# Performance work log

Hardware: AMD Instinct MI355X
Metric: run time of the kernel (lower is better)

The kernel has to match this reference:

```python
import jax, jax.numpy as jnp
import numpy as np

K_MAX = 3
ITERS = 3
NEG_BIG = -1e9


def squash(x):
    # x: [..., O]
    sn = jnp.sum(jnp.square(x), axis=-1, keepdims=True)
    factor = sn / (1.0 + sn) / jnp.sqrt(sn + 1e-8)
    return factor * x


def setup_inputs() -> dict:
    key = jax.random.key(0)
    k1, k2, k3, k4 = jax.random.split(key, 4)
    N, L, D, O = 4096, 200, 64, 64
    behavior_embs = jax.random.normal(k1, (N, L, D), dtype=jnp.float32)
    W = jax.random.normal(k2, (D, O), dtype=jnp.float32)  # init_std=1.0
    routing_logits_init = jax.random.normal(k3, (N, K_MAX, L), dtype=jnp.float32)
    seq_len = jax.random.randint(k4, (N, 1), 0, L, dtype=jnp.int32)
    return {
        "behavior_embs": behavior_embs,
        "W": W,
        "routing_logits_init": routing_logits_init,
        "seq_len": seq_len,
    }


def reference(behavior_embs, W, routing_logits_init, seq_len):
    N, L, D = behavior_embs.shape
    # mask: [N, K_MAX, L] -- valid positions along L, tiled across capsules
    mask = jnp.arange(L)[None, None, :] < seq_len[:, None, :]  # [N,1,L]
    mask = jnp.broadcast_to(mask, (N, K_MAX, L))

    mappings = jnp.matmul(behavior_embs, W)          # [N, L, O]
    m_det = jax.lax.stop_gradient(mappings)         # routing uses detached mappings

    logits = routing_logits_init                     # [N, K_MAX, L]
    for _ in range(ITERS - 1):
        padded = jnp.where(mask, logits, NEG_BIG)
        # NOTE: softmax over the capsule dim (axis=1), as in the original
        weights = jax.nn.softmax(padded, axis=1)     # [N, K_MAX, L]
        candidates = jnp.matmul(weights, m_det)      # [N, K_MAX, O]
        interests = squash(candidates)
        logits = logits + jnp.einsum('nko,nlo->nkl', interests, m_det)

    padded = jnp.where(mask, logits, NEG_BIG)
    weights = jax.nn.softmax(padded, axis=1)
    candidates = jnp.matmul(weights, mappings)       # final iter uses non-detached
    interests = squash(candidates)                   # [N, K_MAX, O]
    return interests
```

## Files before the change

kernel.cpp:

```cpp
#include <hip/hip_runtime.h>
#include <math.h>

typedef _Float16 f16;
typedef _Float16 f16x8 __attribute__((ext_vector_type(8)));
typedef float f32x4 __attribute__((ext_vector_type(4)));

#define LSEQ 200
#define LT 13
#define LKS 7
#define WSTRIDE 224
#define ISTRIDE 80

__global__ __launch_bounds__(256, 4)
void capsule_kernel(const float* __restrict__ E,
                    const float* __restrict__ W,
                    const float* __restrict__ RL,
                    const int* __restrict__ SL,
                    float* __restrict__ out)
{
    __shared__ f16 m_sw[LT*2*64*8];
    __shared__ f16 w_c[3*WSTRIDE];
    __shared__ f16 i_c[3*ISTRIDE];
    __shared__ float logits[3*LSEQ];
    __shared__ float cand[3*64];

    const int n = blockIdx.x;
    const int t = threadIdx.x;
    const int lane = t & 63;
    const int wv = t >> 6;
    const int q = lane >> 4;
    const int cc = lane & 15;

    const int o_own = wv*16 + cc;
    f16x8 wB[2];
    #pragma unroll
    for (int ks = 0; ks < 2; ks++) {
        f16x8 h;
        #pragma unroll
        for (int j = 0; j < 8; j++) h[j] = (f16)W[(ks*32 + q*8 + j)*64 + o_own];
        wB[ks] = h;
    }

    const float4 f4z = make_float4(0.f, 0.f, 0.f, 0.f);

    const float* Eb = E + (size_t)n * (LSEQ*64);
    for (int g = t; g < LT*2*64; g += 256) {
        int sb = g >> 6, c = g & 63;
        int Tl = sb >> 1, ks = sb & 1;
        int qq = c >> 4, m = c & 15;
        int l = Tl*16 + m;
        int kb = ks*32 + qq*8;
        float4 v0 = f4z, v1 = f4z;
        if (l < LSEQ) {
            v0 = *(const float4*)(Eb + l*64 + kb);
            v1 = *(const float4*)(Eb + l*64 + kb + 4);
        }
        f16x8 h = { (f16)v0.x,(f16)v0.y,(f16)v0.z,(f16)v0.w,
                    (f16)v1.x,(f16)v1.y,(f16)v1.z,(f16)v1.w };
        *(f16x8*)&m_sw[g*8] = h;
    }

    if (t < 150) {
        float4 v = *(const float4*)(RL + (size_t)n * 600 + t*4);
        *(float4*)&logits[t*4] = v;
    }
    const int s = SL[n];

    __syncthreads();

    f32x4 acc[LT];
    #pragma unroll
    for (int Tl = 0; Tl < LT; Tl++) {
        f32x4 c0 = {0.f, 0.f, 0.f, 0.f};
        #pragma unroll
        for (int ks = 0; ks < 2; ks++) {
            f16x8 a = *(f16x8*)&m_sw[((Tl*2 + ks)*64 + lane)*8];
            c0 = __builtin_amdgcn_mfma_f32_16x16x32_f16(a, wB[ks], c0, 0, 0, 0);
        }
        acc[Tl] = c0;
    }
    __syncthreads();

    const int kso = o_own >> 5, qo = (o_own & 31) >> 3, jo = o_own & 7;
    #pragma unroll
    for (int Tl = 0; Tl < LT; Tl++) {
        #pragma unroll
        for (int r = 0; r < 4; r++) {
            int lp = q*4 + r;
            m_sw[((Tl*2 + kso)*64 + qo*16 + lp)*8 + jo] = (f16)acc[Tl][r];
        }
    }
    __syncthreads();

    f16x8 mfrag[LKS];
    #pragma unroll
    for (int ks = 0; ks < LKS; ks++) {
        f16x8 h;
        #pragma unroll
        for (int j = 0; j < 8; j++) {
            int l = ks*32 + q*8 + j;
            f16 v = (f16)0.f;
            if (l < 208) {
                int Tl = l >> 4, lp = l & 15;
                v = m_sw[((Tl*2 + kso)*64 + qo*16 + lp)*8 + jo];
            }
            h[j] = v;
        }
        mfrag[ks] = h;
    }

    if (t < LSEQ) {
        float w0, w1, w2;
        if (t < s) {
            float l0 = logits[t], l1 = logits[LSEQ + t], l2 = logits[2*LSEQ + t];
            float mx = fmaxf(fmaxf(l0, l1), l2);
            float e0 = expf(l0 - mx), e1 = expf(l1 - mx), e2 = expf(l2 - mx);
            float inv = 1.f / (e0 + e1 + e2);
            w0 = e0*inv; w1 = e1*inv; w2 = e2*inv;
        } else {
            w0 = w1 = w2 = (1.f/3.f);
        }
        w_c[t]             = (f16)w0;
        w_c[WSTRIDE + t]   = (f16)w1;
        w_c[2*WSTRIDE + t] = (f16)w2;
    }
    __syncthreads();

    const f16x8 hz = {(f16)0.f,(f16)0.f,(f16)0.f,(f16)0.f,
                      (f16)0.f,(f16)0.f,(f16)0.f,(f16)0.f};

    for (int iter = 0; iter < 3; iter++) {
        f32x4 ca = {0.f, 0.f, 0.f, 0.f};
        #pragma unroll
        for (int ks = 0; ks < LKS; ks++) {
            f16x8 b = hz;
            if (cc < 3) b = *(f16x8*)&w_c[cc*WSTRIDE + ks*32 + q*8];
            ca = __builtin_amdgcn_mfma_f32_16x16x32_f16(mfrag[ks], b, ca, 0, 0, 0);
        }
        if (cc < 3) {
            #pragma unroll
            for (int r = 0; r < 4; r++) cand[cc*64 + wv*16 + q*4 + r] = ca[r];
        }
        __syncthreads();

        if (t < 192) {
            float x = cand[t];
            float sq = x*x;
            #pragma unroll
            for (int off = 32; off >= 1; off >>= 1) sq += __shfl_xor(sq, off, 64);
            float factor = sq / ((1.f + sq) * sqrtf(sq + 1e-8f));
            float y = factor * x;
            if (iter < 2) {
                int k = t >> 6, o = t & 63;
                i_c[k*ISTRIDE + o] = (f16)y;
            } else {
                out[(size_t)n*192 + t] = y;
            }
        }
        if (iter == 2) break;
        __syncthreads();

        for (int Tn = wv; Tn < LT; Tn += 4) {
            f32x4 da = {0.f, 0.f, 0.f, 0.f};
            #pragma unroll
            for (int ko = 0; ko < 2; ko++) {
                f16x8 a = hz;
                if (cc < 3) a = *(f16x8*)&i_c[cc*ISTRIDE + ko*32 + q*8];
                f16x8 b = *(f16x8*)&m_sw[((Tn*2 + ko)*64 + lane)*8];
                da = __builtin_amdgcn_mfma_f32_16x16x32_f16(a, b, da, 0, 0, 0);
            }
            if (lane < 16) {
                int l = Tn*16 + lane;
                if (l < LSEQ) {
                    float w0, w1, w2;
                    if (l < s) {
                        float l0 = logits[l]          + da[0];
                        float l1 = logits[LSEQ + l]   + da[1];
                        float l2 = logits[2*LSEQ + l] + da[2];
                        logits[l] = l0; logits[LSEQ + l] = l1; logits[2*LSEQ + l] = l2;
                        float mx = fmaxf(fmaxf(l0, l1), l2);
                        float e0 = expf(l0 - mx), e1 = expf(l1 - mx), e2 = expf(l2 - mx);
                        float inv = 1.f / (e0 + e1 + e2);
                        w0 = e0*inv; w1 = e1*inv; w2 = e2*inv;
                    } else {
                        w0 = w1 = w2 = (1.f/3.f);
                    }
                    w_c[l]             = (f16)w0;
                    w_c[WSTRIDE + l]   = (f16)w1;
                    w_c[2*WSTRIDE + l] = (f16)w2;
                }
            }
        }
        __syncthreads();
    }
}

extern "C" void kernel_launch(void* const* d_in, const int* in_sizes, int n_in,
                              void* d_out, int out_size, void* d_ws, size_t ws_size,
                              hipStream_t stream) {
    const float* E  = (const float*)d_in[0];
    const float* W  = (const float*)d_in[1];
    const float* RL = (const float*)d_in[2];
    const int*   SL = (const int*)d_in[3];
    float* o = (float*)d_out;
    const int N = in_sizes[3];
    capsule_kernel<<<dim3(N), dim3(256), 0, stream>>>(E, W, RL, SL, o);
}
```

Baseline: 314.6 us.

## Keep routing logits in registers and raise occupancy to five blocks per CU

```diff
diff --git a/kernel.cpp b/kernel.cpp
--- a/kernel.cpp
+++ b/kernel.cpp
@@ -7,22 +7,18 @@
 
 #define LSEQ 200
 #define LT 13
-#define LKS 7
-#define WSTRIDE 224
-#define ISTRIDE 80
-
-__global__ __launch_bounds__(256, 4)
+
+__global__ __launch_bounds__(256, 5)
 void capsule_kernel(const float* __restrict__ E,
                     const float* __restrict__ W,
                     const float* __restrict__ RL,
                     const int* __restrict__ SL,
                     float* __restrict__ out)
 {
-    __shared__ f16 m_sw[LT*2*64*8];
-    __shared__ f16 w_c[3*WSTRIDE];
-    __shared__ f16 i_c[3*ISTRIDE];
-    __shared__ float logits[3*LSEQ];
-    __shared__ float cand[3*64];
+    __shared__ f16 m_sw[1792*8];
+    __shared__ f16 w_c[3*224];
+    __shared__ f16 i_c[3*80];
+    __shared__ float cand[192];
 
     const int n = blockIdx.x;
     const int t = threadIdx.x;
@@ -30,6 +26,7 @@
     const int wv = t >> 6;
     const int q = lane >> 4;
     const int cc = lane & 15;
+    const int cmin = cc < 3 ? cc : 2;
 
     const int o_own = wv*16 + cc;
     f16x8 wB[2];
@@ -41,10 +38,33 @@
         wB[ks] = h;
     }
 
+    float lg[4][3];
+    #pragma unroll
+    for (int slot = 0; slot < 4; slot++) {
+        int Tn = wv + slot*4;
+        if (Tn < LT && lane < 16) {
+            int l = Tn*16 + lane;
+            if (l < LSEQ) {
+                lg[slot][0] = RL[(size_t)n*600 + l];
+                lg[slot][1] = RL[(size_t)n*600 + 200 + l];
+                lg[slot][2] = RL[(size_t)n*600 + 400 + l];
+            }
+        }
+    }
+    const int s = SL[n];
+
+    if (t < 9) {
+        const f16x8 hz = {(f16)0.f,(f16)0.f,(f16)0.f,(f16)0.f,
+                          (f16)0.f,(f16)0.f,(f16)0.f,(f16)0.f};
+        int row = t / 3, off = 200 + (t % 3)*8;
+        *(f16x8*)&w_c[row*224 + off] = hz;
+    }
+
+    const float* Eb = E + (size_t)n * (LSEQ*64);
     const float4 f4z = make_float4(0.f, 0.f, 0.f, 0.f);
-
-    const float* Eb = E + (size_t)n * (LSEQ*64);
-    for (int g = t; g < LT*2*64; g += 256) {
+    #pragma unroll
+    for (int i = 0; i < 7; i++) {
+        int g = t + i*256;
         int sb = g >> 6, c = g & 63;
         int Tl = sb >> 1, ks = sb & 1;
         int qq = c >> 4, m = c & 15;
@@ -60,12 +80,6 @@
         *(f16x8*)&m_sw[g*8] = h;
     }
 
-    if (t < 150) {
-        float4 v = *(const float4*)(RL + (size_t)n * 600 + t*4);
-        *(float4*)&logits[t*4] = v;
-    }
-    const int s = SL[n];
-
     __syncthreads();
 
     f32x4 acc[LT];
@@ -90,11 +104,33 @@
             m_sw[((Tl*2 + kso)*64 + qo*16 + lp)*8 + jo] = (f16)acc[Tl][r];
         }
     }
+    #pragma unroll
+    for (int slot = 0; slot < 4; slot++) {
+        int Tn = wv + slot*4;
+        if (Tn < LT && lane < 16) {
+            int l = Tn*16 + lane;
+            if (l < LSEQ) {
+                float w0, w1, w2;
+                if (l < s) {
+                    float l0 = lg[slot][0], l1 = lg[slot][1], l2 = lg[slot][2];
+                    float mx = fmaxf(fmaxf(l0, l1), l2);
+                    float e0 = expf(l0 - mx), e1 = expf(l1 - mx), e2 = expf(l2 - mx);
+                    float inv = 1.f / (e0 + e1 + e2);
+                    w0 = e0*inv; w1 = e1*inv; w2 = e2*inv;
+                } else {
+                    w0 = w1 = w2 = (1.f/3.f);
+                }
+                w_c[l]       = (f16)w0;
+                w_c[224 + l] = (f16)w1;
+                w_c[448 + l] = (f16)w2;
+            }
+        }
+    }
     __syncthreads();
 
-    f16x8 mfrag[LKS];
-    #pragma unroll
-    for (int ks = 0; ks < LKS; ks++) {
+    f16x8 mfrag[7];
+    #pragma unroll
+    for (int ks = 0; ks < 7; ks++) {
         f16x8 h;
         #pragma unroll
         for (int j = 0; j < 8; j++) {
@@ -109,32 +145,11 @@
         mfrag[ks] = h;
     }
 
-    if (t < LSEQ) {
-        float w0, w1, w2;
-        if (t < s) {
-            float l0 = logits[t], l1 = logits[LSEQ + t], l2 = logits[2*LSEQ + t];
-            float mx = fmaxf(fmaxf(l0, l1), l2);
-            float e0 = expf(l0 - mx), e1 = expf(l1 - mx), e2 = expf(l2 - mx);
-            float inv = 1.f / (e0 + e1 + e2);
-            w0 = e0*inv; w1 = e1*inv; w2 = e2*inv;
-        } else {
-            w0 = w1 = w2 = (1.f/3.f);
-        }
-        w_c[t]             = (f16)w0;
-        w_c[WSTRIDE + t]   = (f16)w1;
-        w_c[2*WSTRIDE + t] = (f16)w2;
-    }
-    __syncthreads();
-
-    const f16x8 hz = {(f16)0.f,(f16)0.f,(f16)0.f,(f16)0.f,
-                      (f16)0.f,(f16)0.f,(f16)0.f,(f16)0.f};
-
     for (int iter = 0; iter < 3; iter++) {
         f32x4 ca = {0.f, 0.f, 0.f, 0.f};
         #pragma unroll
-        for (int ks = 0; ks < LKS; ks++) {
-            f16x8 b = hz;
-            if (cc < 3) b = *(f16x8*)&w_c[cc*WSTRIDE + ks*32 + q*8];
+        for (int ks = 0; ks < 7; ks++) {
+            f16x8 b = *(f16x8*)&w_c[cmin*224 + ks*32 + q*8];
             ca = __builtin_amdgcn_mfma_f32_16x16x32_f16(mfrag[ks], b, ca, 0, 0, 0);
         }
         if (cc < 3) {
@@ -151,8 +166,7 @@
             float factor = sq / ((1.f + sq) * sqrtf(sq + 1e-8f));
             float y = factor * x;
             if (iter < 2) {
-                int k = t >> 6, o = t & 63;
-                i_c[k*ISTRIDE + o] = (f16)y;
+                i_c[(t >> 6)*80 + (t & 63)] = (f16)y;
             } else {
                 out[(size_t)n*192 + t] = y;
             }
@@ -160,34 +174,39 @@
         if (iter == 2) break;
         __syncthreads();
 
-        for (int Tn = wv; Tn < LT; Tn += 4) {
-            f32x4 da = {0.f, 0.f, 0.f, 0.f};
-            #pragma unroll
-            for (int ko = 0; ko < 2; ko++) {
-                f16x8 a = hz;
-                if (cc < 3) a = *(f16x8*)&i_c[cc*ISTRIDE + ko*32 + q*8];
-                f16x8 b = *(f16x8*)&m_sw[((Tn*2 + ko)*64 + lane)*8];
-                da = __builtin_amdgcn_mfma_f32_16x16x32_f16(a, b, da, 0, 0, 0);
-            }
-            if (lane < 16) {
-                int l = Tn*16 + lane;
-                if (l < LSEQ) {
-                    float w0, w1, w2;
-                    if (l < s) {
-                        float l0 = logits[l]          + da[0];
-                        float l1 = logits[LSEQ + l]   + da[1];
-                        float l2 = logits[2*LSEQ + l] + da[2];
-                        logits[l] = l0; logits[LSEQ + l] = l1; logits[2*LSEQ + l] = l2;
-                        float mx = fmaxf(fmaxf(l0, l1), l2);
-                        float e0 = expf(l0 - mx), e1 = expf(l1 - mx), e2 = expf(l2 - mx);
-                        float inv = 1.f / (e0 + e1 + e2);
-                        w0 = e0*inv; w1 = e1*inv; w2 = e2*inv;
-                    } else {
-                        w0 = w1 = w2 = (1.f/3.f);
+        f16x8 ia[2];
+        ia[0] = *(f16x8*)&i_c[cmin*80 + q*8];
+        ia[1] = *(f16x8*)&i_c[cmin*80 + 32 + q*8];
+        #pragma unroll
+        for (int slot = 0; slot < 4; slot++) {
+            int Tn = wv + slot*4;
+            if (Tn < LT) {
+                f32x4 da = {0.f, 0.f, 0.f, 0.f};
+                #pragma unroll
+                for (int ko = 0; ko < 2; ko++) {
+                    f16x8 b = *(f16x8*)&m_sw[((Tn*2 + ko)*64 + lane)*8];
+                    da = __builtin_amdgcn_mfma_f32_16x16x32_f16(ia[ko], b, da, 0, 0, 0);
+                }
+                if (lane < 16) {
+                    int l = Tn*16 + lane;
+                    if (l < LSEQ) {
+                        float w0, w1, w2;
+                        if (l < s) {
+                            float l0 = lg[slot][0] + da[0];
+                            float l1 = lg[slot][1] + da[1];
+                            float l2 = lg[slot][2] + da[2];
+                            lg[slot][0] = l0; lg[slot][1] = l1; lg[slot][2] = l2;
+                            float mx = fmaxf(fmaxf(l0, l1), l2);
+                            float e0 = expf(l0 - mx), e1 = expf(l1 - mx), e2 = expf(l2 - mx);
+                            float inv = 1.f / (e0 + e1 + e2);
+                            w0 = e0*inv; w1 = e1*inv; w2 = e2*inv;
+                        } else {
+                            w0 = w1 = w2 = (1.f/3.f);
+                        }
+                        w_c[l]       = (f16)w0;
+                        w_c[224 + l] = (f16)w1;
+                        w_c[448 + l] = (f16)w2;
                     }
-                    w_c[l]             = (f16)w0;
-                    w_c[WSTRIDE + l]   = (f16)w1;
-                    w_c[2*WSTRIDE + l] = (f16)w2;
                 }
             }
         }
```

Measured after the change: 302.5 us. 1.04x faster.
